# Performance work log

Measured on AMD Instinct MI355X. Metric: run time of the kernel, lower is better.

## Reference

```python
import jax, jax.numpy as jnp
import numpy as np


def _hippo_dplr(n):
    # HiPPO-LegS -> NPLR -> DPLR (diagonal plus low rank) init, as in S4
    pr = np.sqrt(1.0 + 2.0 * np.arange(n))
    A = -(np.tril(pr[:, None] * pr[None, :]) - np.diag(np.arange(n)))
    p = np.sqrt(np.arange(n) + 0.5)
    b = np.sqrt(2.0 * np.arange(n) + 1.0)
    S = A + p[:, None] * p[None, :]
    lam_re = np.full(n, np.mean(np.diagonal(S)))
    lam_im, V = np.linalg.eigh(S * -1j)  # S*-1j is Hermitian
    p_c = V.conj().T @ p.astype(np.complex128)
    b_c = V.conj().T @ b.astype(np.complex128)
    return lam_re, lam_im, p_c, b_c


def setup_inputs():
    B, L, H, N = 4, 1024, 512, 64
    key = jax.random.key(0)
    kx, kc, ks, k1, k2 = jax.random.split(key, 5)
    lam_re, lam_im, p_c, b_c = _hippo_dplr(N)
    c = jax.random.normal(kc, (N, 2)) * (0.5 ** 0.5)
    f32 = lambda a: jnp.asarray(a, dtype=jnp.float32)
    return {
        'x': jax.random.normal(kx, (B, L, H), dtype=jnp.float32),
        'norm_weight': jnp.ones((H,), jnp.float32),
        'norm_bias': jnp.zeros((H,), jnp.float32),
        'lambda_re': f32(lam_re), 'lambda_im': f32(lam_im),
        'p_re': f32(p_c.real), 'p_im': f32(p_c.imag),
        'b_re': f32(b_c.real), 'b_im': f32(b_c.imag),
        'c_re': c[:, 0].astype(jnp.float32), 'c_im': c[:, 1].astype(jnp.float32),
        'd': jnp.ones((), jnp.float32),
        'log_step': jax.random.uniform(ks, (), jnp.float32, float(np.log(0.001)), float(np.log(0.1))),
        'out_w': (jax.random.normal(k1, (H, H), jnp.float32) / np.sqrt(H)).astype(jnp.float32),
        'out_b': jnp.zeros((H,), jnp.float32),
        'out2_w': (jax.random.normal(k2, (H, H), jnp.float32) / np.sqrt(H)).astype(jnp.float32),
        'out2_b': jnp.zeros((H,), jnp.float32),
    }


def reference(x, norm_weight, norm_bias, lambda_re, lambda_im, p_re, p_im,
              b_re, b_im, c_re, c_im, d, log_step, out_w, out_b, out2_w, out2_b):
    Bsz, L, H = x.shape
    skip = x
    # LayerNorm over channel dim (eps=1e-5, eqx default)
    mu = jnp.mean(x, -1, keepdims=True)
    var = jnp.mean((x - mu) ** 2, -1, keepdims=True)
    xn = (x - mu) / jnp.sqrt(var + 1e-5) * norm_weight + norm_bias
    # --- S4 DPLR bilinear discretization ---
    lam = (lambda_re + 1j * lambda_im).astype(jnp.complex64)
    p = (p_re + 1j * p_im).astype(jnp.complex64)
    b = (b_re + 1j * b_im).astype(jnp.complex64)
    c = (c_re + 1j * c_im).astype(jnp.complex64)
    step = jnp.exp(log_step).astype(jnp.complex64)
    N = lam.shape[0]
    I = jnp.eye(N, dtype=jnp.complex64)
    A = jnp.diag(lam) - p[:, None] * p[None, :].conj()
    A0 = (2.0 / step) * I + A
    Dinv = jnp.diag(1.0 / ((2.0 / step) - lam))
    qcD = p.conj()[None, :] @ Dinv           # [1,N]
    Dp = Dinv @ p[:, None]                   # [N,1]
    A1 = Dinv - (Dp @ qcD) / (1.0 + (qcD @ p[:, None]))  # Woodbury
    Ab = A1 @ A0                             # [N,N] discrete state matrix
    Bb = 2.0 * (A1 @ b[:, None])[:, 0]       # [N]
    # --- sequential state-space scan over time, vectorized over (B,H) lanes ---
    u = xn.astype(jnp.complex64)             # [B,L,H]

    def step_fn(state, u_t):                 # state: [B,H,N], u_t: [B,H]
        new = jnp.einsum('nm,bhm->bhn', Ab, state) + u_t[..., None] * Bb
        return new, jnp.einsum('n,bhn->bh', c, new).real

    init = jnp.zeros((Bsz, H, N), jnp.complex64)
    _, ys = jax.lax.scan(step_fn, init, jnp.moveaxis(u, 1, 0))  # ys: [L,B,H]
    y = jnp.moveaxis(ys, 0, 1) + d * xn      # feedthrough term
    # --- GELU + GLU-style gated output projection, residual ---
    y = jax.nn.gelu(y)
    gate = jax.nn.sigmoid(y @ out2_w.T + out2_b)
    return skip + (y @ out_w.T + out_b) * gate
```

## Files before the change

### kernel.cpp

```cpp
#include <hip/hip_runtime.h>
#include <hip/hip_bf16.h>
#include <math.h>

#define HDIM 512
#define LSEQ 1024
#define BSZ  4

typedef __attribute__((ext_vector_type(8))) short short8;
typedef __attribute__((ext_vector_type(4))) float floatx4;

__device__ __forceinline__ float2 cmul(float2 a, float2 b) {
  float2 r;
  r.x = a.x * b.x - a.y * b.y;
  r.y = a.x * b.y + a.y * b.x;
  return r;
}
__device__ __forceinline__ float2 cadd(float2 a, float2 b) {
  float2 r; r.x = a.x + b.x; r.y = a.y + b.y; return r;
}
__device__ __forceinline__ float2 cfma(float2 a, float2 b, float2 c) {
  c.x += a.x * b.x - a.y * b.y;
  c.y += a.x * b.y + a.y * b.x;
  return c;
}
__device__ __forceinline__ ushort f2bf(float f) {
  __hip_bfloat16 h = __float2bfloat16(f);
  return *(ushort*)&h;
}

__global__ __launch_bounds__(576) void stage1_kernel(
    const float* __restrict__ x, const float* __restrict__ nw,
    const float* __restrict__ nb, float* __restrict__ xn,
    const float* __restrict__ lre, const float* __restrict__ lim,
    const float* __restrict__ pre, const float* __restrict__ pim,
    const float* __restrict__ bre, const float* __restrict__ bim,
    const float* __restrict__ cre, const float* __restrict__ cim,
    const float* __restrict__ logstep, float* __restrict__ Kout) {
  __shared__ float2 Ldab[64], Lu[64], Lr[64], LBb[64];
  __shared__ float2 Rv[2048];
  __shared__ float2 Wv[2048];
  int tid = threadIdx.x;
  int wv = tid >> 6;
  int lane = tid & 63;

  if (blockIdx.x != 0) {
    int row = (blockIdx.x - 1) * 9 + wv;
    if (row >= BSZ * LSEQ) return;
    const float* xr = x + (size_t)row * HDIM;
    float4 v0 = ((const float4*)xr)[lane];
    float4 v1 = ((const float4*)xr)[lane + 64];
    float s  = v0.x + v0.y + v0.z + v0.w + v1.x + v1.y + v1.z + v1.w;
    float ss = v0.x*v0.x + v0.y*v0.y + v0.z*v0.z + v0.w*v0.w
             + v1.x*v1.x + v1.y*v1.y + v1.z*v1.z + v1.w*v1.w;
    #pragma unroll
    for (int m = 1; m < 64; m <<= 1) { s += __shfl_xor(s, m); ss += __shfl_xor(ss, m); }
    float mu   = s * (1.0f / HDIM);
    float var  = ss * (1.0f / HDIM) - mu * mu;
    float rstd = rsqrtf(var + 1e-5f);
    float4 w0 = ((const float4*)nw)[lane];
    float4 w1 = ((const float4*)nw)[lane + 64];
    float4 b0 = ((const float4*)nb)[lane];
    float4 b1 = ((const float4*)nb)[lane + 64];
    float4 o0, o1;
    o0.x = (v0.x - mu) * rstd * w0.x + b0.x;
    o0.y = (v0.y - mu) * rstd * w0.y + b0.y;
    o0.z = (v0.z - mu) * rstd * w0.z + b0.z;
    o0.w = (v0.w - mu) * rstd * w0.w + b0.w;
    o1.x = (v1.x - mu) * rstd * w1.x + b1.x;
    o1.y = (v1.y - mu) * rstd * w1.y + b1.y;
    o1.z = (v1.z - mu) * rstd * w1.z + b1.z;
    o1.w = (v1.w - mu) * rstd * w1.w + b1.w;
    float* xo = xn + (size_t)row * HDIM;
    ((float4*)xo)[lane] = o0;
    ((float4*)xo)[lane + 64] = o1;
    return;
  }

  if (tid < 64) {
    int n = tid;
    float step = expf(logstep[0]);
    float g = 2.0f / step;
    float lr = lre[n], li = lim[n];
    float pr = pre[n], pi = pim[n];
    float br = bre[n], bi = bim[n];
    float den  = (g - lr) * (g - lr) + li * li;
    float dinr = (g - lr) / den, dini = li / den;
    float dabr = (g + lr) * dinr - li * dini;
    float dabi = (g + lr) * dini + li * dinr;
    float ur = dinr * pr - dini * pi;
    float ui = dinr * pi + dini * pr;
    float qr = pr * dinr + pi * dini;
    float qi = pr * dini - pi * dinr;
    float pm2 = pr * pr + pi * pi;
    float betr = pm2 * dinr, beti = pm2 * dini;
    float gar = qr * br - qi * bi;
    float gai = qr * bi + qi * br;
    #pragma unroll
    for (int m = 1; m < 64; m <<= 1) {
      betr += __shfl_xor(betr, m); beti += __shfl_xor(beti, m);
      gar  += __shfl_xor(gar, m);  gai  += __shfl_xor(gai, m);
    }
    float obr = 1.0f + betr, obi = beti;
    float ob2 = obr * obr + obi * obi;
    float kr = -2.0f * g * obr / ob2;
    float ki =  2.0f * g * obi / ob2;
    float rr = kr * qr - ki * qi;
    float ri = kr * qi + ki * qr;
    float tgr = (gar * obr + gai * obi) / ob2;
    float tgi = (gai * obr - gar * obi) / ob2;
    float dbr = dinr * br - dini * bi;
    float dbi = dinr * bi + dini * br;
    float Bbr = 2.0f * (dbr - (ur * tgr - ui * tgi));
    float Bbi = 2.0f * (dbi - (ur * tgi + ui * tgr));
    float2 t;
    t.x = dabr; t.y = dabi; Ldab[n] = t;
    t.x = ur;   t.y = ui;   Lu[n]   = t;
    t.x = rr;   t.y = ri;   Lr[n]   = t;
    t.x = Bbr;  t.y = Bbi;  LBb[n]  = t;
  }
  if (wv == 8) { float2 cc; cc.x = cre[lane]; cc.y = cim[lane]; Rv[lane] = cc; }
  __syncthreads();

  int g8 = lane >> 3;
  int q8 = lane & 7;
  int jm = wv * 8 + g8;
  float2 cv[8];

  if (wv < 8) {
    float2 dab[8], u[8], rn[8];
    #pragma unroll
    for (int ii = 0; ii < 8; ii++) {
      int n = q8 * 8 + ii;
      dab[ii] = Ldab[n]; u[ii] = Lu[n]; rn[ii] = Lr[n];
    }
    float2 rj = Lr[jm];
    #pragma unroll
    for (int ii = 0; ii < 8; ii++) {
      int n = q8 * 8 + ii;
      cv[ii] = cmul(u[ii], rj);
      if (n == jm) cv[ii] = cadd(cv[ii], dab[ii]);
    }
    for (int s = 0; s < 31; s++) {
      float2 part; part.x = 0.f; part.y = 0.f;
      #pragma unroll
      for (int ii = 0; ii < 8; ii++) part = cfma(rn[ii], cv[ii], part);
      #pragma unroll
      for (int m = 1; m < 8; m <<= 1) {
        part.x += __shfl_xor(part.x, m);
        part.y += __shfl_xor(part.y, m);
      }
      #pragma unroll
      for (int ii = 0; ii < 8; ii++) {
        float2 nc = cmul(dab[ii], cv[ii]);
        cv[ii] = cfma(u[ii], part, nc);
      }
    }
  } else {
    float2 dab0 = Ldab[lane], u0 = Lu[lane], r0 = Lr[lane];
    float2 w = LBb[lane];
    Wv[lane * 32 + 0] = w;
    for (int b = 1; b < 32; b++) {
      float dr = r0.x * w.x - r0.y * w.y;
      float di = r0.x * w.y + r0.y * w.x;
      #pragma unroll
      for (int m = 1; m < 64; m <<= 1) { dr += __shfl_xor(dr, m); di += __shfl_xor(di, m); }
      float2 nw2;
      nw2.x = dab0.x * w.x - dab0.y * w.y + u0.x * dr - u0.y * di;
      nw2.y = dab0.x * w.y + dab0.y * w.x + u0.x * di + u0.y * dr;
      w = nw2;
      Wv[lane * 32 + b] = w;
    }
  }
  __syncthreads();

  for (int a = 1; a < 32; a++) {
    if (wv < 8) {
      float2 part; part.x = 0.f; part.y = 0.f;
      #pragma unroll
      for (int ii = 0; ii < 8; ii++) {
        float2 Rk = Rv[(a - 1) * 64 + q8 * 8 + ii];
        part = cfma(Rk, cv[ii], part);
      }
      #pragma unroll
      for (int m = 1; m < 8; m <<= 1) {
        part.x += __shfl_xor(part.x, m);
        part.y += __shfl_xor(part.y, m);
      }
      if (q8 == 0) Rv[a * 64 + jm] = part;
    }
    __syncthreads();
  }

  for (int midx = tid; midx < 1024; midx += 576) {
    int a = midx >> 5, b = midx & 31;
    float acc = 0.f;
    for (int n = 0; n < 64; n++) {
      float2 R = Rv[a * 64 + n];
      float2 W = Wv[n * 32 + b];
      acc += R.x * W.x - R.y * W.y;
    }
    Kout[midx] = acc;
  }
}

__global__ __launch_bounds__(256) void prep_kernel(
    const float* __restrict__ xn, const float* __restrict__ K,
    const float* __restrict__ w1, const float* __restrict__ w2,
    ushort* __restrict__ Uhi, ushort* __restrict__ Ulo,
    ushort* __restrict__ Thi, ushort* __restrict__ Tlo,
    ushort* __restrict__ Wst) {
  __shared__ float tile[64][65];
  int blk = blockIdx.x;
  int tid = threadIdx.x;
  if (blk < 512) {
    int ht = blk & 7, lt = (blk >> 3) & 15, b = blk >> 7;
    #pragma unroll
    for (int q = 0; q < 16; q++) {
      int idx = q * 256 + tid;
      int r = idx >> 6, c = idx & 63;
      tile[r][c] = xn[((size_t)(b * LSEQ + lt * 64 + r)) * HDIM + ht * 64 + c];
    }
    __syncthreads();
    #pragma unroll
    for (int q = 0; q < 16; q++) {
      int idx = q * 256 + tid;
      int r = idx >> 6, c = idx & 63;
      float v = tile[c][r];
      ushort h = f2bf(v);
      float rem = v - __bfloat162float(*(__hip_bfloat16*)&h);
      ushort l = f2bf(rem);
      size_t off = ((size_t)(b * HDIM + ht * 64 + r)) * LSEQ + lt * 64 + c;
      Uhi[off] = h;
      Ulo[off] = l;
    }
  } else if (blk < 768) {
    int e0 = ((blk - 512) * 256 + tid) * 8;
    int n = e0 >> 9, k0 = e0 & 511;
    const float* Wr = (n < 512) ? (w1 + (size_t)n * 512 + k0)
                                : (w2 + (size_t)(n - 512) * 512 + k0);
    ushort tmp[8];
    #pragma unroll
    for (int t = 0; t < 8; t++) tmp[t] = f2bf(Wr[t]);
    *(short8*)&Wst[e0] = *(short8*)tmp;
  } else {
    int r = blk - 768;
    int t = r * 2 + (tid >> 7);
    int tau0 = (tid & 127) * 8;
    ushort hi[8], lo[8];
    #pragma unroll
    for (int q = 0; q < 8; q++) {
      int tau = tau0 + q;
      float v = (tau <= t) ? K[t - tau] : 0.f;
      hi[q] = f2bf(v);
      float rem = v - __bfloat162float(*(__hip_bfloat16*)&hi[q]);
      lo[q] = f2bf(rem);
    }
    *(short8*)&Thi[(size_t)t * 1024 + tau0] = *(short8*)hi;
    *(short8*)&Tlo[(size_t)t * 1024 + tau0] = *(short8*)lo;
  }
}

__global__ __launch_bounds__(256) void conv_gemm_kernel(
    const ushort* __restrict__ Thi, const ushort* __restrict__ Tlo,
    const ushort* __restrict__ Uhi, const ushort* __restrict__ Ulo,
    const float* __restrict__ xn, const float* __restrict__ dptr,
    __hip_bfloat16* __restrict__ A) {
  __shared__ ushort sTh[64 * 40];
  __shared__ ushort sTl[64 * 40];
  __shared__ ushort sUh[64 * 40];
  __shared__ ushort sUl[64 * 40];
  int tid = threadIdx.x;
  int lane = tid & 63;
  int wv = tid >> 6;
  int wm = wv >> 1, wn = wv & 1;
  int by = blockIdx.y;
  int bm = (by < 8) ? by : 23 - by;
  int bn = blockIdx.x;
  floatx4 acc[2][2] = {};
  int srow = tid >> 2;
  int scol = (tid & 3) * 8;
  int fr = lane & 15, fq = (lane >> 4) * 8;
  size_t Toff = (size_t)(bm * 64 + srow) * 1024 + scol;
  size_t Uoff = (size_t)(bn * 64 + srow) * 1024 + scol;
  int KT = 2 * (bm + 1);
  for (int kt = 0; kt < KT; kt++) {
    int k0 = kt * 32;
    *(uint4*)&sTh[srow * 40 + scol] = *(const uint4*)&Thi[Toff + k0];
    *(uint4*)&sTl[srow * 40 + scol] = *(const uint4*)&Tlo[Toff + k0];
    *(uint4*)&sUh[srow * 40 + scol] = *(const uint4*)&Uhi[Uoff + k0];
    *(uint4*)&sUl[srow * 40 + scol] = *(const uint4*)&Ulo[Uoff + k0];
    __syncthreads();
    short8 ah[2], al[2], bh[2], bl[2];
    #pragma unroll
    for (int i = 0; i < 2; i++) {
      ah[i] = *(const short8*)&sTh[(wm * 32 + i * 16 + fr) * 40 + fq];
      al[i] = *(const short8*)&sTl[(wm * 32 + i * 16 + fr) * 40 + fq];
      bh[i] = *(const short8*)&sUh[(wn * 32 + i * 16 + fr) * 40 + fq];
      bl[i] = *(const short8*)&sUl[(wn * 32 + i * 16 + fr) * 40 + fq];
    }
    #pragma unroll
    for (int i = 0; i < 2; i++)
      #pragma unroll
      for (int j = 0; j < 2; j++) {
        acc[i][j] = __builtin_amdgcn_mfma_f32_16x16x32_bf16(ah[i], bh[j], acc[i][j], 0, 0, 0);
        acc[i][j] = __builtin_amdgcn_mfma_f32_16x16x32_bf16(al[i], bh[j], acc[i][j], 0, 0, 0);
        acc[i][j] = __builtin_amdgcn_mfma_f32_16x16x32_bf16(ah[i], bl[j], acc[i][j], 0, 0, 0);
      }
    __syncthreads();
  }
  float d = dptr[0];
  int row0 = bm * 64 + wm * 32;
  int col0 = bn * 64 + wn * 32;
  int fc = lane & 15, frq = (lane >> 4) * 4;
  #pragma unroll
  for (int i = 0; i < 2; i++)
    #pragma unroll
    for (int j = 0; j < 2; j++)
      #pragma unroll
      for (int r = 0; r < 4; r++) {
        int t = row0 + i * 16 + frq + r;
        int c = col0 + j * 16 + fc;
        int b = c >> 9, h = c & 511;
        size_t off = (size_t)(b * LSEQ + t) * HDIM + h;
        float y = acc[i][j][r] + d * xn[off];
        float tnh = tanhf(0.7978845608028654f * (y + 0.044715f * y * y * y));
        A[off] = __float2bfloat16(0.5f * y * (1.0f + tnh));
      }
}

__global__ __launch_bounds__(256) void proj_kernel(
    const __hip_bfloat16* __restrict__ Abuf, const ushort* __restrict__ Wst,
    const float* __restrict__ x, const float* __restrict__ ob,
    const float* __restrict__ o2b, float* __restrict__ out) {
  __shared__ ushort sA[64 * 40];
  __shared__ ushort sW1[64 * 40];
  __shared__ ushort sW2[64 * 40];
  int tid = threadIdx.x;
  int lane = tid & 63;
  int wv = tid >> 6;
  int wm = wv >> 1, wn = wv & 1;
  int bm = blockIdx.y, bn = blockIdx.x;
  int srow = tid >> 2;
  int scol = (tid & 3) * 8;
  int fr = lane & 15, fq = (lane >> 4) * 8;
  floatx4 acc1[2][2] = {}, acc2[2][2] = {};
  const ushort* Ab = (const ushort*)Abuf;
  size_t Aoff  = (size_t)(bm * 64 + srow) * 512 + scol;
  size_t W1off = (size_t)(bn * 64 + srow) * 512 + scol;
  size_t W2off = W1off + (size_t)512 * 512;
  for (int kt = 0; kt < 16; kt++) {
    int k0 = kt * 32;
    *(uint4*)&sA[srow * 40 + scol]  = *(const uint4*)&Ab[Aoff + k0];
    *(uint4*)&sW1[srow * 40 + scol] = *(const uint4*)&Wst[W1off + k0];
    *(uint4*)&sW2[srow * 40 + scol] = *(const uint4*)&Wst[W2off + k0];
    __syncthreads();
    short8 af[2], b1[2], b2[2];
    #pragma unroll
    for (int i = 0; i < 2; i++) {
      af[i] = *(const short8*)&sA[(wm * 32 + i * 16 + fr) * 40 + fq];
      b1[i] = *(const short8*)&sW1[(wn * 32 + i * 16 + fr) * 40 + fq];
      b2[i] = *(const short8*)&sW2[(wn * 32 + i * 16 + fr) * 40 + fq];
    }
    #pragma unroll
    for (int i = 0; i < 2; i++)
      #pragma unroll
      for (int j = 0; j < 2; j++) {
        acc1[i][j] = __builtin_amdgcn_mfma_f32_16x16x32_bf16(af[i], b1[j], acc1[i][j], 0, 0, 0);
        acc2[i][j] = __builtin_amdgcn_mfma_f32_16x16x32_bf16(af[i], b2[j], acc2[i][j], 0, 0, 0);
      }
    __syncthreads();
  }
  int row0 = bm * 64 + wm * 32;
  int col0 = bn * 64 + wn * 32;
  int fc = lane & 15, frq = (lane >> 4) * 4;
  #pragma unroll
  for (int i = 0; i < 2; i++)
    #pragma unroll
    for (int j = 0; j < 2; j++)
      #pragma unroll
      for (int r = 0; r < 4; r++) {
        int row = row0 + i * 16 + frq + r;
        int col = col0 + j * 16 + fc;
        float c1 = acc1[i][j][r] + ob[col];
        float c2 = acc2[i][j][r] + o2b[col];
        float gate = 1.0f / (1.0f + expf(-c2));
        size_t off = (size_t)row * HDIM + col;
        out[off] = x[off] + c1 * gate;
      }
}

extern "C" void kernel_launch(void* const* d_in, const int* in_sizes, int n_in,
                              void* d_out, int out_size, void* d_ws, size_t ws_size,
                              hipStream_t stream) {
  const float* x   = (const float*)d_in[0];
  const float* nw  = (const float*)d_in[1];
  const float* nb  = (const float*)d_in[2];
  const float* lre = (const float*)d_in[3];
  const float* lim = (const float*)d_in[4];
  const float* pre = (const float*)d_in[5];
  const float* pim = (const float*)d_in[6];
  const float* bre = (const float*)d_in[7];
  const float* bim = (const float*)d_in[8];
  const float* cre = (const float*)d_in[9];
  const float* cim = (const float*)d_in[10];
  const float* dsc = (const float*)d_in[11];
  const float* lst = (const float*)d_in[12];
  const float* w1  = (const float*)d_in[13];
  const float* ob  = (const float*)d_in[14];
  const float* w2  = (const float*)d_in[15];
  const float* o2b = (const float*)d_in[16];

  char* ws = (char*)d_ws;
  float* xn    = (float*)(ws);
  ushort* Uhi  = (ushort*)(ws + (size_t)(8  << 20));
  ushort* Ulo  = (ushort*)(ws + (size_t)(12 << 20));
  ushort* Thi  = (ushort*)(ws + (size_t)(16 << 20));
  ushort* Tlo  = (ushort*)(ws + (size_t)(18 << 20));
  ushort* Wst  = (ushort*)(ws + (size_t)(20 << 20));
  __hip_bfloat16* Abuf = (__hip_bfloat16*)(ws + (size_t)(21 << 20));
  float* Kbuf  = (float*)(ws + (size_t)(25 << 20));
  float* out   = (float*)d_out;

  stage1_kernel<<<dim3(457), dim3(576), 0, stream>>>(x, nw, nb, xn,
                                                     lre, lim, pre, pim, bre, bim,
                                                     cre, cim, lst, Kbuf);
  prep_kernel<<<dim3(1280), dim3(256), 0, stream>>>(xn, Kbuf, w1, w2,
                                                    Uhi, Ulo, Thi, Tlo, Wst);
  conv_gemm_kernel<<<dim3(32, 16), dim3(256), 0, stream>>>(Thi, Tlo, Uhi, Ulo,
                                                           xn, dsc, Abuf);
  proj_kernel<<<dim3(8, 64), dim3(256), 0, stream>>>(Abuf, Wst, x, ob, o2b, out);
}
```

Baseline: 172.1 us.

## Double-buffer LDS tiles in GEMMs and move weight bf16 cast into stage1

The conv and projection GEMM kernels now use double-buffered shared memory. Global loads for the next K-tile are issued into registers before the MFMAs on the current tile and stored to the alternate buffer afterwards, which removes one barrier per iteration and hides load latency. Separately, the fp32→bf16 conversion of the output weights moves from prep_kernel into the otherwise idle threads of the stage1 LayerNorm blocks, shrinking prep's grid. The cost is double the LDS per block, which can lower occupancy, plus more live registers.

```diff
diff --git a/kernel.cpp b/kernel.cpp
--- a/kernel.cpp
+++ b/kernel.cpp
@@ -35,7 +35,9 @@
     const float* __restrict__ pre, const float* __restrict__ pim,
     const float* __restrict__ bre, const float* __restrict__ bim,
     const float* __restrict__ cre, const float* __restrict__ cim,
-    const float* __restrict__ logstep, float* __restrict__ Kout) {
+    const float* __restrict__ logstep, float* __restrict__ Kout,
+    const float* __restrict__ w1, const float* __restrict__ w2,
+    ushort* __restrict__ Wst) {
   __shared__ float2 Ldab[64], Lu[64], Lr[64], LBb[64];
   __shared__ float2 Rv[2048];
   __shared__ float2 Wv[2048];
@@ -45,34 +47,46 @@
 
   if (blockIdx.x != 0) {
     int row = (blockIdx.x - 1) * 9 + wv;
-    if (row >= BSZ * LSEQ) return;
-    const float* xr = x + (size_t)row * HDIM;
-    float4 v0 = ((const float4*)xr)[lane];
-    float4 v1 = ((const float4*)xr)[lane + 64];
-    float s  = v0.x + v0.y + v0.z + v0.w + v1.x + v1.y + v1.z + v1.w;
-    float ss = v0.x*v0.x + v0.y*v0.y + v0.z*v0.z + v0.w*v0.w
-             + v1.x*v1.x + v1.y*v1.y + v1.z*v1.z + v1.w*v1.w;
-    #pragma unroll
-    for (int m = 1; m < 64; m <<= 1) { s += __shfl_xor(s, m); ss += __shfl_xor(ss, m); }
-    float mu   = s * (1.0f / HDIM);
-    float var  = ss * (1.0f / HDIM) - mu * mu;
-    float rstd = rsqrtf(var + 1e-5f);
-    float4 w0 = ((const float4*)nw)[lane];
-    float4 w1 = ((const float4*)nw)[lane + 64];
-    float4 b0 = ((const float4*)nb)[lane];
-    float4 b1 = ((const float4*)nb)[lane + 64];
-    float4 o0, o1;
-    o0.x = (v0.x - mu) * rstd * w0.x + b0.x;
-    o0.y = (v0.y - mu) * rstd * w0.y + b0.y;
-    o0.z = (v0.z - mu) * rstd * w0.z + b0.z;
-    o0.w = (v0.w - mu) * rstd * w0.w + b0.w;
-    o1.x = (v1.x - mu) * rstd * w1.x + b1.x;
-    o1.y = (v1.y - mu) * rstd * w1.y + b1.y;
-    o1.z = (v1.z - mu) * rstd * w1.z + b1.z;
-    o1.w = (v1.w - mu) * rstd * w1.w + b1.w;
-    float* xo = xn + (size_t)row * HDIM;
-    ((float4*)xo)[lane] = o0;
-    ((float4*)xo)[lane + 64] = o1;
+    if (row < BSZ * LSEQ) {
+      const float* xr = x + (size_t)row * HDIM;
+      float4 v0 = ((const float4*)xr)[lane];
+      float4 v1 = ((const float4*)xr)[lane + 64];
+      float s  = v0.x + v0.y + v0.z + v0.w + v1.x + v1.y + v1.z + v1.w;
+      float ss = v0.x*v0.x + v0.y*v0.y + v0.z*v0.z + v0.w*v0.w
+               + v1.x*v1.x + v1.y*v1.y + v1.z*v1.z + v1.w*v1.w;
+      #pragma unroll
+      for (int m = 1; m < 64; m <<= 1) { s += __shfl_xor(s, m); ss += __shfl_xor(ss, m); }
+      float mu   = s * (1.0f / HDIM);
+      float var  = ss * (1.0f / HDIM) - mu * mu;
+      float rstd = rsqrtf(var + 1e-5f);
+      float4 w0 = ((const float4*)nw)[lane];
+      float4 w1v = ((const float4*)nw)[lane + 64];
+      float4 b0 = ((const float4*)nb)[lane];
+      float4 b1 = ((const float4*)nb)[lane + 64];
+      float4 o0, o1;
+      o0.x = (v0.x - mu) * rstd * w0.x + b0.x;
+      o0.y = (v0.y - mu) * rstd * w0.y + b0.y;
+      o0.z = (v0.z - mu) * rstd * w0.z + b0.z;
+      o0.w = (v0.w - mu) * rstd * w0.w + b0.w;
+      o1.x = (v1.x - mu) * rstd * w1v.x + b1.x;
+      o1.y = (v1.y - mu) * rstd * w1v.y + b1.y;
+      o1.z = (v1.z - mu) * rstd * w1v.z + b1.z;
+      o1.w = (v1.w - mu) * rstd * w1v.w + b1.w;
+      float* xo = xn + (size_t)row * HDIM;
+      ((float4*)xo)[lane] = o0;
+      ((float4*)xo)[lane + 64] = o1;
+    }
+    int idx = (blockIdx.x - 1) * 576 + tid;
+    if (idx < 65536) {
+      int e0 = idx * 8;
+      int n = e0 >> 9, k0 = e0 & 511;
+      const float* Wr = (n < 512) ? (w1 + (size_t)n * 512 + k0)
+                                  : (w2 + (size_t)(n - 512) * 512 + k0);
+      ushort tmp[8];
+      #pragma unroll
+      for (int q = 0; q < 8; q++) tmp[q] = f2bf(Wr[q]);
+      *(short8*)&Wst[e0] = *(short8*)tmp;
+    }
     return;
   }
 
@@ -205,10 +219,8 @@
 
 __global__ __launch_bounds__(256) void prep_kernel(
     const float* __restrict__ xn, const float* __restrict__ K,
-    const float* __restrict__ w1, const float* __restrict__ w2,
     ushort* __restrict__ Uhi, ushort* __restrict__ Ulo,
-    ushort* __restrict__ Thi, ushort* __restrict__ Tlo,
-    ushort* __restrict__ Wst) {
+    ushort* __restrict__ Thi, ushort* __restrict__ Tlo) {
   __shared__ float tile[64][65];
   int blk = blockIdx.x;
   int tid = threadIdx.x;
@@ -233,17 +245,8 @@
       Uhi[off] = h;
       Ulo[off] = l;
     }
-  } else if (blk < 768) {
-    int e0 = ((blk - 512) * 256 + tid) * 8;
-    int n = e0 >> 9, k0 = e0 & 511;
-    const float* Wr = (n < 512) ? (w1 + (size_t)n * 512 + k0)
-                                : (w2 + (size_t)(n - 512) * 512 + k0);
-    ushort tmp[8];
-    #pragma unroll
-    for (int t = 0; t < 8; t++) tmp[t] = f2bf(Wr[t]);
-    *(short8*)&Wst[e0] = *(short8*)tmp;
   } else {
-    int r = blk - 768;
+    int r = blk - 512;
     int t = r * 2 + (tid >> 7);
     int tau0 = (tid & 127) * 8;
     ushort hi[8], lo[8];
@@ -265,10 +268,7 @@
     const ushort* __restrict__ Uhi, const ushort* __restrict__ Ulo,
     const float* __restrict__ xn, const float* __restrict__ dptr,
     __hip_bfloat16* __restrict__ A) {
-  __shared__ ushort sTh[64 * 40];
-  __shared__ ushort sTl[64 * 40];
-  __shared__ ushort sUh[64 * 40];
-  __shared__ ushort sUl[64 * 40];
+  __shared__ ushort sbuf[2 * 10240];
   int tid = threadIdx.x;
   int lane = tid & 63;
   int wv = tid >> 6;
@@ -279,17 +279,36 @@
   floatx4 acc[2][2] = {};
   int srow = tid >> 2;
   int scol = (tid & 3) * 8;
+  int ldst = srow * 40 + scol;
   int fr = lane & 15, fq = (lane >> 4) * 8;
   size_t Toff = (size_t)(bm * 64 + srow) * 1024 + scol;
   size_t Uoff = (size_t)(bn * 64 + srow) * 1024 + scol;
   int KT = 2 * (bm + 1);
+  {
+    uint4 th = *(const uint4*)&Thi[Toff];
+    uint4 tl = *(const uint4*)&Tlo[Toff];
+    uint4 uh = *(const uint4*)&Uhi[Uoff];
+    uint4 ul = *(const uint4*)&Ulo[Uoff];
+    *(uint4*)&sbuf[ldst]        = th;
+    *(uint4*)&sbuf[ldst + 2560] = tl;
+    *(uint4*)&sbuf[ldst + 5120] = uh;
+    *(uint4*)&sbuf[ldst + 7680] = ul;
+  }
+  __syncthreads();
   for (int kt = 0; kt < KT; kt++) {
-    int k0 = kt * 32;
-    *(uint4*)&sTh[srow * 40 + scol] = *(const uint4*)&Thi[Toff + k0];
-    *(uint4*)&sTl[srow * 40 + scol] = *(const uint4*)&Tlo[Toff + k0];
-    *(uint4*)&sUh[srow * 40 + scol] = *(const uint4*)&Uhi[Uoff + k0];
-    *(uint4*)&sUl[srow * 40 + scol] = *(const uint4*)&Ulo[Uoff + k0];
-    __syncthreads();
+    int cur = kt & 1;
+    uint4 nth = {}, ntl = {}, nuh = {}, nul = {};
+    if (kt + 1 < KT) {
+      size_t k1 = (size_t)(kt + 1) * 32;
+      nth = *(const uint4*)&Thi[Toff + k1];
+      ntl = *(const uint4*)&Tlo[Toff + k1];
+      nuh = *(const uint4*)&Uhi[Uoff + k1];
+      nul = *(const uint4*)&Ulo[Uoff + k1];
+    }
+    const ushort* sTh = sbuf + cur * 10240;
+    const ushort* sTl = sTh + 2560;
+    const ushort* sUh = sTh + 5120;
+    const ushort* sUl = sTh + 7680;
     short8 ah[2], al[2], bh[2], bl[2];
     #pragma unroll
     for (int i = 0; i < 2; i++) {
@@ -306,7 +325,14 @@
         acc[i][j] = __builtin_amdgcn_mfma_f32_16x16x32_bf16(al[i], bh[j], acc[i][j], 0, 0, 0);
         acc[i][j] = __builtin_amdgcn_mfma_f32_16x16x32_bf16(ah[i], bl[j], acc[i][j], 0, 0, 0);
       }
-    __syncthreads();
+    if (kt + 1 < KT) {
+      ushort* dst = sbuf + (cur ^ 1) * 10240;
+      *(uint4*)&dst[ldst]        = nth;
+      *(uint4*)&dst[ldst + 2560] = ntl;
+      *(uint4*)&dst[ldst + 5120] = nuh;
+      *(uint4*)&dst[ldst + 7680] = nul;
+      __syncthreads();
+    }
   }
   float d = dptr[0];
   int row0 = bm * 64 + wm * 32;
@@ -332,9 +358,7 @@
     const __hip_bfloat16* __restrict__ Abuf, const ushort* __restrict__ Wst,
     const float* __restrict__ x, const float* __restrict__ ob,
     const float* __restrict__ o2b, float* __restrict__ out) {
-  __shared__ ushort sA[64 * 40];
-  __shared__ ushort sW1[64 * 40];
-  __shared__ ushort sW2[64 * 40];
+  __shared__ ushort sbuf[2 * 7680];
   int tid = threadIdx.x;
   int lane = tid & 63;
   int wv = tid >> 6;
@@ -342,18 +366,34 @@
   int bm = blockIdx.y, bn = blockIdx.x;
   int srow = tid >> 2;
   int scol = (tid & 3) * 8;
+  int ldst = srow * 40 + scol;
   int fr = lane & 15, fq = (lane >> 4) * 8;
   floatx4 acc1[2][2] = {}, acc2[2][2] = {};
   const ushort* Ab = (const ushort*)Abuf;
   size_t Aoff  = (size_t)(bm * 64 + srow) * 512 + scol;
   size_t W1off = (size_t)(bn * 64 + srow) * 512 + scol;
   size_t W2off = W1off + (size_t)512 * 512;
+  {
+    uint4 a0 = *(const uint4*)&Ab[Aoff];
+    uint4 v1 = *(const uint4*)&Wst[W1off];
+    uint4 v2 = *(const uint4*)&Wst[W2off];
+    *(uint4*)&sbuf[ldst]        = a0;
+    *(uint4*)&sbuf[ldst + 2560] = v1;
+    *(uint4*)&sbuf[ldst + 5120] = v2;
+  }
+  __syncthreads();
   for (int kt = 0; kt < 16; kt++) {
-    int k0 = kt * 32;
-    *(uint4*)&sA[srow * 40 + scol]  = *(const uint4*)&Ab[Aoff + k0];
-    *(uint4*)&sW1[srow * 40 + scol] = *(const uint4*)&Wst[W1off + k0];
-    *(uint4*)&sW2[srow * 40 + scol] = *(const uint4*)&Wst[W2off + k0];
-    __syncthreads();
+    int cur = kt & 1;
+    uint4 na = {}, n1 = {}, n2 = {};
+    if (kt + 1 < 16) {
+      int k1 = (kt + 1) * 32;
+      na = *(const uint4*)&Ab[Aoff + k1];
+      n1 = *(const uint4*)&Wst[W1off + k1];
+      n2 = *(const uint4*)&Wst[W2off + k1];
+    }
+    const ushort* sA  = sbuf + cur * 7680;
+    const ushort* sW1 = sA + 2560;
+    const ushort* sW2 = sA + 5120;
     short8 af[2], b1[2], b2[2];
     #pragma unroll
     for (int i = 0; i < 2; i++) {
@@ -368,7 +408,13 @@
         acc1[i][j] = __builtin_amdgcn_mfma_f32_16x16x32_bf16(af[i], b1[j], acc1[i][j], 0, 0, 0);
         acc2[i][j] = __builtin_amdgcn_mfma_f32_16x16x32_bf16(af[i], b2[j], acc2[i][j], 0, 0, 0);
       }
-    __syncthreads();
+    if (kt + 1 < 16) {
+      ushort* dst = sbuf + (cur ^ 1) * 7680;
+      *(uint4*)&dst[ldst]        = na;
+      *(uint4*)&dst[ldst + 2560] = n1;
+      *(uint4*)&dst[ldst + 5120] = n2;
+      __syncthreads();
+    }
   }
   int row0 = bm * 64 + wm * 32;
   int col0 = bn * 64 + wn * 32;
@@ -423,9 +469,9 @@
 
   stage1_kernel<<<dim3(457), dim3(576), 0, stream>>>(x, nw, nb, xn,
                                                      lre, lim, pre, pim, bre, bim,
-                                                     cre, cim, lst, Kbuf);
-  prep_kernel<<<dim3(1280), dim3(256), 0, stream>>>(xn, Kbuf, w1, w2,
-                                                    Uhi, Ulo, Thi, Tlo, Wst);
+                                                     cre, cim, lst, Kbuf,
+                                                     w1, w2, Wst);
+  prep_kernel<<<dim3(1024), dim3(256), 0, stream>>>(xn, Kbuf, Uhi, Ulo, Thi, Tlo);
   conv_gemm_kernel<<<dim3(32, 16), dim3(256), 0, stream>>>(Thi, Tlo, Uhi, Ulo,
                                                            xn, dsc, Abuf);
   proj_kernel<<<dim3(8, 64), dim3(256), 0, stream>>>(Abuf, Wst, x, ob, o2b, out);
```

Result: no change. 170.0 us (-1.2%).
